# Kernel optimization log

Hardware: AMD Instinct MI355X
Metric: run time of the kernel (lower is better)

Reference implementation:

```python
import jax, jax.numpy as jnp
import numpy as np

N_SERIES = 4096
MAX_STEP = 2
NUM_MATS = 2 * MAX_STEP + 1  # len(supports)*K + 1


def setup_inputs() -> dict:
    key = jax.random.key(0)
    ks = jax.random.split(key, 6)
    B, N, C, D, O = 4, N_SERIES, 2, 64, 64
    F = C + D  # 66
    scale = 1.0 / jnp.sqrt(jnp.float32(N))  # keep diffusion powers numerically sane
    xavier = jnp.sqrt(2.0 / (F * NUM_MATS + O)).astype(jnp.float32)
    return {
        "inputs": jax.random.normal(ks[0], (B, N * C), dtype=jnp.float32),
        "state": jax.random.normal(ks[1], (B, N * D), dtype=jnp.float32),
        "support0": jax.random.normal(ks[2], (N, N), dtype=jnp.float32) * scale,
        "support1": jax.random.normal(ks[3], (N, N), dtype=jnp.float32) * scale,
        "weight": jax.random.normal(ks[4], (F * NUM_MATS, O), dtype=jnp.float32) * xavier,
        "biases": jnp.zeros((O,), dtype=jnp.float32),
        "output_size": 64,
    }


def reference(inputs, state, support0, support1, weight, biases, output_size):
    B = inputs.shape[0]
    N = N_SERIES
    x_in = inputs.reshape(B, N, -1)
    h_in = state.reshape(B, N, -1)
    xs = jnp.concatenate([x_in, h_in], axis=2)  # [B, N, F]
    F = xs.shape[2]
    # (N, F, B) -> (N, F*B), matching torch permute(1,2,0).reshape
    x0 = jnp.transpose(xs, (1, 2, 0)).reshape(N, F * B)
    mats = [x0]
    # Faithful to source: x0 is mutated inside the loop and carries over
    # between supports (the Chebyshev recurrence quirk of the original).
    for support in (support0, support1):
        x1 = support @ x0
        mats.append(x1)
        for _ in range(2, MAX_STEP + 1):
            x2 = 2.0 * (support @ x1) - x0
            mats.append(x2)
            x1, x0 = x2, x1
    x = jnp.stack(mats, axis=0)  # [num_mats, N, F*B]
    x = x.reshape(NUM_MATS, N, F, B)
    x = jnp.transpose(x, (3, 1, 2, 0))  # [B, N, F, num_mats]
    x = x.reshape(B * N, F * NUM_MATS)
    out = x @ weight + biases  # [B*N, O]
    return out.reshape(B, N * output_size)
```

## Files before the change

kernel.cpp:

```cpp
#include <hip/hip_runtime.h>
#include <stdint.h>

typedef unsigned short u16;
typedef u16 u16x4 __attribute__((ext_vector_type(4)));
typedef u16 u16x8 __attribute__((ext_vector_type(8)));
typedef __bf16 bf16x8 __attribute__((ext_vector_type(8)));
typedef float f32x4 __attribute__((ext_vector_type(4)));

#define NSER 4096
#define KDIM 4096
#define NCOLS 288
#define MATSZ (NCOLS * NSER)
#define PE ((size_t)NCOLS * NSER)

__device__ __forceinline__ u16 f2bf(float f) {
  uint32_t u = __builtin_bit_cast(uint32_t, f);
  u += 0x7FFFu + ((u >> 16) & 1u);
  return (u16)(u >> 16);
}
__device__ __forceinline__ float bf2f(u16 h) {
  return __builtin_bit_cast(float, (uint32_t)h << 16);
}

typedef const void __attribute__((address_space(1)))* gas1p;
typedef void __attribute__((address_space(3)))* las3p;

__device__ __forceinline__ void gload16(const void* g, void* l) {
  __builtin_amdgcn_global_load_lds((gas1p)g, (las3p)l, 16, 0, 0);
}

__global__ __launch_bounds__(256) void k_build_x(const float* __restrict__ inputs,
                                                 const float* __restrict__ state,
                                                 u16* __restrict__ xb) {
  __shared__ float tile[64][65];
  const int nt = blockIdx.x, b = blockIdx.y;
  const int n0 = nt * 64;
  const int t = threadIdx.x;
  {
    const int i = t >> 2;
    const int c0 = (t & 3) * 16;
    const float* sp = state + ((int64_t)b * NSER + (n0 + i)) * 64 + c0;
    #pragma unroll
    for (int q = 0; q < 4; ++q) {
      float4 v = *(const float4*)(sp + q * 4);
      tile[i][c0 + q * 4 + 0] = v.x;
      tile[i][c0 + q * 4 + 1] = v.y;
      tile[i][c0 + q * 4 + 2] = v.z;
      tile[i][c0 + q * 4 + 3] = v.w;
    }
  }
  __syncthreads();
  const int wv = t >> 6, lane = t & 63;
  #pragma unroll
  for (int it = 0; it < 16; ++it) {
    const int d = wv + 4 * it;
    xb[(size_t)((2 + d) * 4 + b) * NSER + n0 + lane] = f2bf(tile[lane][d]);
  }
  if (t < 128) {
    const int c = t >> 6, j = t & 63;
    xb[(size_t)(c * 4 + b) * NSER + n0 + j] =
        f2bf(inputs[(int64_t)b * (NSER * 2) + (int64_t)(n0 + j) * 2 + c]);
  }
  if (b == 0) {
    for (int idx = t; idx < 24 * 64; idx += 256)
      xb[(size_t)(264 + idx / 64) * NSER + n0 + (idx & 63)] = 0;
  }
}

#define BM 64
#define BN 288
#define BK 64
#define KC 4
#define ABYTES (BM * BK * 2)
#define BBYTES (BN * BK * 2)
#define BUFSZ  (ABYTES + BBYTES)

__global__ __launch_bounds__(256) void k_gemm(const float* __restrict__ A0f,
                                              const float* __restrict__ A1f,
                                              const u16* __restrict__ Bm,
                                              float* __restrict__ Pb) {
  int kc = blockIdx.z;
  const float* Af = A0f;
  if (kc >= KC) { Af = A1f; kc -= KC; }
  const int i0 = blockIdx.x * BM;
  const int t = threadIdx.x;
  const int wid = t >> 6, lane = t & 63;
  const int NKT = KDIM / KC / BK;
  const int k0 = kc * (KDIM / KC);

  __shared__ char smem[2 * BUFSZ];

  int a_grow[2], a_ldst[2];
  #pragma unroll
  for (int s = 0; s < 2; ++s) {
    const int row = (wid * 2 + s) * 8 + (lane >> 3);
    a_grow[s] = row * KDIM + (lane & 7) * 8;
    a_ldst[s] = row * 128 + 16 * ((lane & 7) ^ (row & 7));
  }
  int b_src[9];
  #pragma unroll
  for (int s = 0; s < 9; ++s) {
    const int row = (wid * 9 + s) * 8 + (lane >> 3);
    b_src[s] = row * (KDIM * 2) + 16 * ((lane & 7) ^ (row & 7));
  }
  const float* Ag = Af + (int64_t)i0 * KDIM + k0;
  const char* Bg = (const char*)Bm + (int64_t)k0 * 2;

  int aoffs[2], axors[2];
  #pragma unroll
  for (int mf = 0; mf < 2; ++mf) {
    const int row = (wid >> 1) * 32 + mf * 16 + (lane & 15);
    aoffs[mf] = row * 128;
    axors[mf] = (row & 7) << 4;
  }
  int boffs[9], bxors[9];
  #pragma unroll
  for (int nf = 0; nf < 9; ++nf) {
    const int row = (wid & 1) * 144 + nf * 16 + (lane & 15);
    boffs[nf] = ABYTES + row * 128;
    bxors[nf] = (row & 7) << 4;
  }
  const int klane = (lane >> 4) * 16;

  f32x4 acc[2][9];
  #pragma unroll
  for (int mf = 0; mf < 2; ++mf)
    #pragma unroll
    for (int nf = 0; nf < 9; ++nf)
      acc[mf][nf] = (f32x4){0.f, 0.f, 0.f, 0.f};

  f32x4 areg[2][2];

  #pragma unroll
  for (int s = 0; s < 2; ++s) {
    areg[s][0] = *(const f32x4*)(Ag + a_grow[s]);
    areg[s][1] = *(const f32x4*)(Ag + a_grow[s] + 4);
  }
  #pragma unroll
  for (int s = 0; s < 9; ++s)
    gload16(Bg + b_src[s], smem + ABYTES + (wid * 9 + s) * 1024);
  #pragma unroll
  for (int s = 0; s < 2; ++s) {
    u16x8 w;
    #pragma unroll
    for (int q = 0; q < 4; ++q) { w[q] = f2bf(areg[s][0][q]); w[4 + q] = f2bf(areg[s][1][q]); }
    *(u16x8*)(smem + a_ldst[s]) = w;
  }
  __syncthreads();

  for (int kt = 0; kt < NKT; ++kt) {
    const int cur = kt & 1;
    char* sbuf = smem + (cur ^ 1) * BUFSZ;
    if (kt + 1 < NKT) {
      const float* Ak = Ag + (kt + 1) * BK;
      const char* Bk = Bg + (kt + 1) * (BK * 2);
      #pragma unroll
      for (int s = 0; s < 2; ++s) {
        areg[s][0] = *(const f32x4*)(Ak + a_grow[s]);
        areg[s][1] = *(const f32x4*)(Ak + a_grow[s] + 4);
      }
      #pragma unroll
      for (int s = 0; s < 9; ++s)
        gload16(Bk + b_src[s], sbuf + ABYTES + (wid * 9 + s) * 1024);
    }
    __builtin_amdgcn_sched_barrier(0);
    const char* sb = smem + cur * BUFSZ;
    #pragma unroll
    for (int kk = 0; kk < 2; ++kk) {
      const int kb = kk * 64 + klane;
      bf16x8 af[2];
      #pragma unroll
      for (int mf = 0; mf < 2; ++mf)
        af[mf] = *(const bf16x8*)(sb + aoffs[mf] + (kb ^ axors[mf]));
      #pragma unroll
      for (int nf = 0; nf < 9; ++nf) {
        bf16x8 bv = *(const bf16x8*)(sb + boffs[nf] + (kb ^ bxors[nf]));
        #pragma unroll
        for (int mf = 0; mf < 2; ++mf)
          acc[mf][nf] = __builtin_amdgcn_mfma_f32_16x16x32_bf16(af[mf], bv,
                                                                acc[mf][nf], 0, 0, 0);
      }
    }
    __builtin_amdgcn_sched_barrier(0);
    if (kt + 1 < NKT) {
      #pragma unroll
      for (int s = 0; s < 2; ++s) {
        u16x8 w;
        #pragma unroll
        for (int q = 0; q < 4; ++q) { w[q] = f2bf(areg[s][0][q]); w[4 + q] = f2bf(areg[s][1][q]); }
        *(u16x8*)(sbuf + a_ldst[s]) = w;
      }
    }
    __syncthreads();
  }

  float* Pp = Pb + (size_t)blockIdx.z * PE;
  #pragma unroll
  for (int mf = 0; mf < 2; ++mf) {
    const int i = i0 + (wid >> 1) * 32 + mf * 16 + ((lane >> 4) << 2);
    #pragma unroll
    for (int nf = 0; nf < 9; ++nf) {
      const int j = (wid & 1) * 144 + nf * 16 + (lane & 15);
      *(f32x4*)(Pp + (size_t)j * NSER + i) = acc[mf][nf];
    }
  }
}

__global__ __launch_bounds__(256) void k_reduce(const float* __restrict__ P,
                                                u16* __restrict__ o) {
  const size_t i = ((size_t)blockIdx.x * 256 + threadIdx.x) * 4;
  f32x4 s = *(const f32x4*)(P + i);
  #pragma unroll
  for (int k = 1; k < 4; ++k)
    s += *(const f32x4*)(P + (size_t)k * PE + i);
  u16x4 w;
  #pragma unroll
  for (int r = 0; r < 4; ++r) w[r] = f2bf(s[r]);
  *(u16x4*)(o + i) = w;
}

__global__ __launch_bounds__(256) void k_final(const float* __restrict__ weight,
                                               const float* __restrict__ biases,
                                               const u16* __restrict__ Xb,
                                               const u16* __restrict__ m1b,
                                               const u16* __restrict__ m3b,
                                               const float* __restrict__ P,
                                               float* __restrict__ out) {
  __shared__ float w2[330][32];
  const int nt = blockIdx.x, b = blockIdx.y, oh = blockIdx.z;
  const int n0 = nt * 64;
  const int t = threadIdx.x;
  const int lane = t & 63, wv = t >> 6;
  {
    const int ol = t & 31;
    const int o = oh * 32 + ol;
    for (int f = t >> 5; f < 66; f += 8) {
      const float v0 = weight[(f * 5 + 0) * 64 + o];
      const float v1 = weight[(f * 5 + 1) * 64 + o];
      const float v2 = weight[(f * 5 + 2) * 64 + o];
      const float v3 = weight[(f * 5 + 3) * 64 + o];
      const float v4 = weight[(f * 5 + 4) * 64 + o];
      w2[f * 5 + 0][ol] = v0 - v2;
      w2[f * 5 + 1][ol] = v1 - v4;
      w2[f * 5 + 2][ol] = 2.f * v2;
      w2[f * 5 + 3][ol] = v3;
      w2[f * 5 + 4][ol] = 2.f * v4;
    }
  }
  __syncthreads();
  const int ob = oh * 32 + wv * 8;
  float acc[8];
  #pragma unroll
  for (int i = 0; i < 8; ++i) acc[i] = biases[ob + i];
  for (int f = 0; f < 66; ++f) {
    const size_t base = (size_t)(f * 4 + b) * NSER + n0 + lane;
    float y[5];
    y[0] = bf2f(Xb[base]);
    y[1] = bf2f(m1b[base]);
    y[2] = P[base] + P[PE + base] + P[2 * PE + base] + P[3 * PE + base];
    y[3] = bf2f(m3b[base]);
    y[4] = P[4 * PE + base] + P[5 * PE + base] + P[6 * PE + base] + P[7 * PE + base];
    #pragma unroll
    for (int mat = 0; mat < 5; ++mat) {
      const float* wr = &w2[f * 5 + mat][wv * 8];
      #pragma unroll
      for (int i = 0; i < 8; ++i) acc[i] = fmaf(y[mat], wr[i], acc[i]);
    }
  }
  float* op = out + (size_t)b * (NSER * 64) + (size_t)(n0 + lane) * 64 + ob;
  #pragma unroll
  for (int i = 0; i < 8; ++i) op[i] = acc[i];
}

extern "C" void kernel_launch(void* const* d_in, const int* in_sizes, int n_in,
                              void* d_out, int out_size, void* d_ws, size_t ws_size,
                              hipStream_t stream) {
  const float* inputs = (const float*)d_in[0];
  const float* state  = (const float*)d_in[1];
  const float* s0     = (const float*)d_in[2];
  const float* s1     = (const float*)d_in[3];
  const float* weight = (const float*)d_in[4];
  const float* biases = (const float*)d_in[5];
  float* out = (float*)d_out;

  char* ws = (char*)d_ws;
  u16* Xb  = (u16*)ws;
  u16* m1b = Xb + MATSZ;
  u16* m3b = m1b + MATSZ;
  float* P = (float*)(ws + (size_t)3 * 2359296);

  k_build_x<<<dim3(64, 4, 1), 256, 0, stream>>>(inputs, state, Xb);
  k_gemm<<<dim3(64, 1, 4), 256, 0, stream>>>(s0, s0, Xb, P);
  k_reduce<<<dim3(1152, 1, 1), 256, 0, stream>>>(P, m1b);
  k_gemm<<<dim3(64, 1, 8), 256, 0, stream>>>(s0, s1, m1b, P);
  k_reduce<<<dim3(1152, 1, 1), 256, 0, stream>>>(P + 4 * PE, m3b);
  k_gemm<<<dim3(64, 1, 4), 256, 0, stream>>>(s1, s1, m3b, P + 4 * PE);
  k_final<<<dim3(64, 4, 2), 256, 0, stream>>>(weight, biases, Xb, m1b, m3b, P, out);
}
```

Measured before the change: 161.9 us.

## Replace LDS-staged GEMM with register-direct MFMA loads and wider split-K

The shared-memory double-buffered GEMM is replaced by a 128-thread kernel where each wave loads its A rows (fp32, converted to bf16) and all 288 B columns straight from global memory into registers, with no LDS or barriers. Split-K goes from 4 to 8 chunks for the first and last GEMMs, adding parallelism. When the workspace is large enough, the middle product is reduced to bf16 in a paired reduce and the last GEMM uses 8 partials, which changes the final kernel's reads. The cost is much heavier global and L2 traffic for B, since there is no LDS reuse across waves, plus extra partial-sum memory.

```diff
diff --git a/kernel.cpp b/kernel.cpp
--- a/kernel.cpp
+++ b/kernel.cpp
@@ -20,13 +20,6 @@
 }
 __device__ __forceinline__ float bf2f(u16 h) {
   return __builtin_bit_cast(float, (uint32_t)h << 16);
-}
-
-typedef const void __attribute__((address_space(1)))* gas1p;
-typedef void __attribute__((address_space(3)))* las3p;
-
-__device__ __forceinline__ void gload16(const void* g, void* l) {
-  __builtin_amdgcn_global_load_lds((gas1p)g, (las3p)l, 16, 0, 0);
 }
 
 __global__ __launch_bounds__(256) void k_build_x(const float* __restrict__ inputs,
@@ -67,151 +60,96 @@
   }
 }
 
-#define BM 64
-#define BN 288
-#define BK 64
-#define KC 4
-#define ABYTES (BM * BK * 2)
-#define BBYTES (BN * BK * 2)
-#define BUFSZ  (ABYTES + BBYTES)
-
-__global__ __launch_bounds__(256) void k_gemm(const float* __restrict__ A0f,
-                                              const float* __restrict__ A1f,
-                                              const u16* __restrict__ Bm,
-                                              float* __restrict__ Pb) {
+template <int KCC>
+__global__ __launch_bounds__(128, 1) void k_gemm(const float* __restrict__ A0f,
+                                                 const float* __restrict__ A1f,
+                                                 const u16* __restrict__ Bm,
+                                                 float* __restrict__ Pb) {
   int kc = blockIdx.z;
   const float* Af = A0f;
-  if (kc >= KC) { Af = A1f; kc -= KC; }
-  const int i0 = blockIdx.x * BM;
-  const int t = threadIdx.x;
-  const int wid = t >> 6, lane = t & 63;
-  const int NKT = KDIM / KC / BK;
-  const int k0 = kc * (KDIM / KC);
-
-  __shared__ char smem[2 * BUFSZ];
-
-  int a_grow[2], a_ldst[2];
+  if (kc >= KCC) { Af = A1f; kc -= KCC; }
+  const int lane = threadIdx.x & 63;
+  const int w = threadIdx.x >> 6;
+  const int i0w = blockIdx.x * 64 + w * 32;
+  const int KCH = KDIM / KCC;
+  const int NK = KCH / 32;
+  const int k0 = kc * KCH;
+
+  const int l15 = lane & 15;
+  const int koff = (lane >> 4) * 8;
+
+  const float* pA0 = Af + (size_t)(i0w + l15) * KDIM + k0 + koff;
+  const float* pA1 = pA0 + (size_t)16 * KDIM;
+  const char* bB = (const char*)Bm + ((size_t)l15 * KDIM + k0 + koff) * 2;
+
+  f32x4 acc[2][18];
+  #pragma unroll
+  for (int s = 0; s < 2; ++s)
+    #pragma unroll
+    for (int nf = 0; nf < 18; ++nf) acc[s][nf] = (f32x4){0.f, 0.f, 0.f, 0.f};
+
+  #pragma unroll 2
+  for (int ks = 0; ks < NK; ++ks) {
+    const int kb = ks * 32;
+    f32x4 a00 = *(const f32x4*)(pA0 + kb);
+    f32x4 a01 = *(const f32x4*)(pA0 + kb + 4);
+    f32x4 a10 = *(const f32x4*)(pA1 + kb);
+    f32x4 a11 = *(const f32x4*)(pA1 + kb + 4);
+    const char* bptr = bB + (size_t)kb * 2;
+    bf16x8 bva[6], bvb[6];
+    #pragma unroll
+    for (int q = 0; q < 6; ++q)
+      bva[q] = *(const bf16x8*)(bptr + (size_t)q * (16 * KDIM * 2));
+    #pragma unroll
+    for (int q = 0; q < 6; ++q)
+      bvb[q] = *(const bf16x8*)(bptr + (size_t)(6 + q) * (16 * KDIM * 2));
+    u16x8 w0, w1;
+    #pragma unroll
+    for (int q = 0; q < 4; ++q) {
+      w0[q] = f2bf(a00[q]); w0[4 + q] = f2bf(a01[q]);
+      w1[q] = f2bf(a10[q]); w1[4 + q] = f2bf(a11[q]);
+    }
+    const bf16x8 af0 = __builtin_bit_cast(bf16x8, w0);
+    const bf16x8 af1 = __builtin_bit_cast(bf16x8, w1);
+    #pragma unroll
+    for (int q = 0; q < 6; ++q) {
+      acc[0][q] = __builtin_amdgcn_mfma_f32_16x16x32_bf16(af0, bva[q], acc[0][q], 0, 0, 0);
+      acc[1][q] = __builtin_amdgcn_mfma_f32_16x16x32_bf16(af1, bva[q], acc[1][q], 0, 0, 0);
+    }
+    #pragma unroll
+    for (int q = 0; q < 6; ++q)
+      bva[q] = *(const bf16x8*)(bptr + (size_t)(12 + q) * (16 * KDIM * 2));
+    #pragma unroll
+    for (int q = 0; q < 6; ++q) {
+      acc[0][6 + q] = __builtin_amdgcn_mfma_f32_16x16x32_bf16(af0, bvb[q], acc[0][6 + q], 0, 0, 0);
+      acc[1][6 + q] = __builtin_amdgcn_mfma_f32_16x16x32_bf16(af1, bvb[q], acc[1][6 + q], 0, 0, 0);
+    }
+    #pragma unroll
+    for (int q = 0; q < 6; ++q) {
+      acc[0][12 + q] = __builtin_amdgcn_mfma_f32_16x16x32_bf16(af0, bva[q], acc[0][12 + q], 0, 0, 0);
+      acc[1][12 + q] = __builtin_amdgcn_mfma_f32_16x16x32_bf16(af1, bva[q], acc[1][12 + q], 0, 0, 0);
+    }
+  }
+
+  float* Pp = Pb + (size_t)blockIdx.z * PE;
   #pragma unroll
   for (int s = 0; s < 2; ++s) {
-    const int row = (wid * 2 + s) * 8 + (lane >> 3);
-    a_grow[s] = row * KDIM + (lane & 7) * 8;
-    a_ldst[s] = row * 128 + 16 * ((lane & 7) ^ (row & 7));
-  }
-  int b_src[9];
-  #pragma unroll
-  for (int s = 0; s < 9; ++s) {
-    const int row = (wid * 9 + s) * 8 + (lane >> 3);
-    b_src[s] = row * (KDIM * 2) + 16 * ((lane & 7) ^ (row & 7));
-  }
-  const float* Ag = Af + (int64_t)i0 * KDIM + k0;
-  const char* Bg = (const char*)Bm + (int64_t)k0 * 2;
-
-  int aoffs[2], axors[2];
-  #pragma unroll
-  for (int mf = 0; mf < 2; ++mf) {
-    const int row = (wid >> 1) * 32 + mf * 16 + (lane & 15);
-    aoffs[mf] = row * 128;
-    axors[mf] = (row & 7) << 4;
-  }
-  int boffs[9], bxors[9];
-  #pragma unroll
-  for (int nf = 0; nf < 9; ++nf) {
-    const int row = (wid & 1) * 144 + nf * 16 + (lane & 15);
-    boffs[nf] = ABYTES + row * 128;
-    bxors[nf] = (row & 7) << 4;
-  }
-  const int klane = (lane >> 4) * 16;
-
-  f32x4 acc[2][9];
-  #pragma unroll
-  for (int mf = 0; mf < 2; ++mf)
-    #pragma unroll
-    for (int nf = 0; nf < 9; ++nf)
-      acc[mf][nf] = (f32x4){0.f, 0.f, 0.f, 0.f};
-
-  f32x4 areg[2][2];
-
-  #pragma unroll
-  for (int s = 0; s < 2; ++s) {
-    areg[s][0] = *(const f32x4*)(Ag + a_grow[s]);
-    areg[s][1] = *(const f32x4*)(Ag + a_grow[s] + 4);
-  }
-  #pragma unroll
-  for (int s = 0; s < 9; ++s)
-    gload16(Bg + b_src[s], smem + ABYTES + (wid * 9 + s) * 1024);
-  #pragma unroll
-  for (int s = 0; s < 2; ++s) {
-    u16x8 w;
-    #pragma unroll
-    for (int q = 0; q < 4; ++q) { w[q] = f2bf(areg[s][0][q]); w[4 + q] = f2bf(areg[s][1][q]); }
-    *(u16x8*)(smem + a_ldst[s]) = w;
-  }
-  __syncthreads();
-
-  for (int kt = 0; kt < NKT; ++kt) {
-    const int cur = kt & 1;
-    char* sbuf = smem + (cur ^ 1) * BUFSZ;
-    if (kt + 1 < NKT) {
-      const float* Ak = Ag + (kt + 1) * BK;
-      const char* Bk = Bg + (kt + 1) * (BK * 2);
-      #pragma unroll
-      for (int s = 0; s < 2; ++s) {
-        areg[s][0] = *(const f32x4*)(Ak + a_grow[s]);
-        areg[s][1] = *(const f32x4*)(Ak + a_grow[s] + 4);
-      }
-      #pragma unroll
-      for (int s = 0; s < 9; ++s)
-        gload16(Bk + b_src[s], sbuf + ABYTES + (wid * 9 + s) * 1024);
-    }
-    __builtin_amdgcn_sched_barrier(0);
-    const char* sb = smem + cur * BUFSZ;
-    #pragma unroll
-    for (int kk = 0; kk < 2; ++kk) {
-      const int kb = kk * 64 + klane;
-      bf16x8 af[2];
-      #pragma unroll
-      for (int mf = 0; mf < 2; ++mf)
-        af[mf] = *(const bf16x8*)(sb + aoffs[mf] + (kb ^ axors[mf]));
-      #pragma unroll
-      for (int nf = 0; nf < 9; ++nf) {
-        bf16x8 bv = *(const bf16x8*)(sb + boffs[nf] + (kb ^ bxors[nf]));
-        #pragma unroll
-        for (int mf = 0; mf < 2; ++mf)
-          acc[mf][nf] = __builtin_amdgcn_mfma_f32_16x16x32_bf16(af[mf], bv,
-                                                                acc[mf][nf], 0, 0, 0);
-      }
-    }
-    __builtin_amdgcn_sched_barrier(0);
-    if (kt + 1 < NKT) {
-      #pragma unroll
-      for (int s = 0; s < 2; ++s) {
-        u16x8 w;
-        #pragma unroll
-        for (int q = 0; q < 4; ++q) { w[q] = f2bf(areg[s][0][q]); w[4 + q] = f2bf(areg[s][1][q]); }
-        *(u16x8*)(sbuf + a_ldst[s]) = w;
-      }
-    }
-    __syncthreads();
-  }
-
-  float* Pp = Pb + (size_t)blockIdx.z * PE;
-  #pragma unroll
-  for (int mf = 0; mf < 2; ++mf) {
-    const int i = i0 + (wid >> 1) * 32 + mf * 16 + ((lane >> 4) << 2);
-    #pragma unroll
-    for (int nf = 0; nf < 9; ++nf) {
-      const int j = (wid & 1) * 144 + nf * 16 + (lane & 15);
-      *(f32x4*)(Pp + (size_t)j * NSER + i) = acc[mf][nf];
-    }
-  }
-}
-
+    const int i = i0w + s * 16 + ((lane >> 4) << 2);
+    #pragma unroll
+    for (int nf = 0; nf < 18; ++nf) {
+      const int j = nf * 16 + l15;
+      *(f32x4*)(Pp + (size_t)j * NSER + i) = acc[s][nf];
+    }
+  }
+}
+
+template <int NS>
 __global__ __launch_bounds__(256) void k_reduce(const float* __restrict__ P,
                                                 u16* __restrict__ o) {
   const size_t i = ((size_t)blockIdx.x * 256 + threadIdx.x) * 4;
   f32x4 s = *(const f32x4*)(P + i);
   #pragma unroll
-  for (int k = 1; k < 4; ++k)
+  for (int k = 1; k < NS; ++k)
     s += *(const f32x4*)(P + (size_t)k * PE + i);
   u16x4 w;
   #pragma unroll
@@ -219,11 +157,29 @@
   *(u16x4*)(o + i) = w;
 }
 
+__global__ __launch_bounds__(256) void k_reduce_pair(const float* __restrict__ P,
+                                                     u16* __restrict__ m2b,
+                                                     u16* __restrict__ m3b) {
+  const float* p = P + (size_t)blockIdx.z * (4 * PE);
+  u16* o = blockIdx.z ? m3b : m2b;
+  const size_t i = ((size_t)blockIdx.x * 256 + threadIdx.x) * 4;
+  f32x4 s = *(const f32x4*)(p + i);
+  #pragma unroll
+  for (int k = 1; k < 4; ++k)
+    s += *(const f32x4*)(p + (size_t)k * PE + i);
+  u16x4 w;
+  #pragma unroll
+  for (int r = 0; r < 4; ++r) w[r] = f2bf(s[r]);
+  *(u16x4*)(o + i) = w;
+}
+
+template <int BIG>
 __global__ __launch_bounds__(256) void k_final(const float* __restrict__ weight,
                                                const float* __restrict__ biases,
                                                const u16* __restrict__ Xb,
                                                const u16* __restrict__ m1b,
                                                const u16* __restrict__ m3b,
+                                               const u16* __restrict__ m2b,
                                                const float* __restrict__ P,
                                                float* __restrict__ out) {
   __shared__ float w2[330][32];
@@ -257,9 +213,17 @@
     float y[5];
     y[0] = bf2f(Xb[base]);
     y[1] = bf2f(m1b[base]);
-    y[2] = P[base] + P[PE + base] + P[2 * PE + base] + P[3 * PE + base];
     y[3] = bf2f(m3b[base]);
-    y[4] = P[4 * PE + base] + P[5 * PE + base] + P[6 * PE + base] + P[7 * PE + base];
+    if (BIG) {
+      y[2] = bf2f(m2b[base]);
+      float s = P[base];
+      #pragma unroll
+      for (int k = 1; k < 8; ++k) s += P[(size_t)k * PE + base];
+      y[4] = s;
+    } else {
+      y[2] = P[base] + P[PE + base] + P[2 * PE + base] + P[3 * PE + base];
+      y[4] = P[4 * PE + base] + P[5 * PE + base] + P[6 * PE + base] + P[7 * PE + base];
+    }
     #pragma unroll
     for (int mat = 0; mat < 5; ++mat) {
       const float* wr = &w2[f * 5 + mat][wv * 8];
@@ -287,13 +251,28 @@
   u16* Xb  = (u16*)ws;
   u16* m1b = Xb + MATSZ;
   u16* m3b = m1b + MATSZ;
-  float* P = (float*)(ws + (size_t)3 * 2359296);
+  const size_t SMALL_P_OFF = (size_t)3 * 2359296;
+  const size_t BIG_P_OFF   = (size_t)4 * 2359296;
+  const bool big = ws_size >= BIG_P_OFF + 8ull * 4718592;
 
   k_build_x<<<dim3(64, 4, 1), 256, 0, stream>>>(inputs, state, Xb);
-  k_gemm<<<dim3(64, 1, 4), 256, 0, stream>>>(s0, s0, Xb, P);
-  k_reduce<<<dim3(1152, 1, 1), 256, 0, stream>>>(P, m1b);
-  k_gemm<<<dim3(64, 1, 8), 256, 0, stream>>>(s0, s1, m1b, P);
-  k_reduce<<<dim3(1152, 1, 1), 256, 0, stream>>>(P + 4 * PE, m3b);
-  k_gemm<<<dim3(64, 1, 4), 256, 0, stream>>>(s1, s1, m3b, P + 4 * PE);
-  k_final<<<dim3(64, 4, 2), 256, 0, stream>>>(weight, biases, Xb, m1b, m3b, P, out);
-}
+
+  if (big) {
+    u16* m2b = m3b + MATSZ;
+    float* P = (float*)(ws + BIG_P_OFF);
+    k_gemm<8><<<dim3(64, 1, 8), 128, 0, stream>>>(s0, s0, Xb, P);
+    k_reduce<8><<<dim3(1152, 1, 1), 256, 0, stream>>>(P, m1b);
+    k_gemm<4><<<dim3(64, 1, 8), 128, 0, stream>>>(s0, s1, m1b, P);
+    k_reduce_pair<<<dim3(1152, 1, 2), 256, 0, stream>>>(P, m2b, m3b);
+    k_gemm<8><<<dim3(64, 1, 8), 128, 0, stream>>>(s1, s1, m3b, P);
+    k_final<1><<<dim3(64, 4, 2), 256, 0, stream>>>(weight, biases, Xb, m1b, m3b, m2b, P, out);
+  } else {
+    float* P = (float*)(ws + SMALL_P_OFF);
+    k_gemm<8><<<dim3(64, 1, 8), 128, 0, stream>>>(s0, s0, Xb, P);
+    k_reduce<8><<<dim3(1152, 1, 1), 256, 0, stream>>>(P, m1b);
+    k_gemm<4><<<dim3(64, 1, 8), 128, 0, stream>>>(s0, s1, m1b, P);
+    k_reduce<4><<<dim3(1152, 1, 1), 256, 0, stream>>>(P + 4 * PE, m3b);
+    k_gemm<4><<<dim3(64, 1, 4), 128, 0, stream>>>(s1, s1, m3b, P + 4 * PE);
+    k_final<0><<<dim3(64, 4, 2), 256, 0, stream>>>(weight, biases, Xb, m1b, m3b, nullptr, P, out);
+  }
+}
```

New measurement: 240.3 us. +48.4%, slower.
